# Kernel optimization log

Hardware: AMD Instinct MI355X
Metric: run time of the kernel (lower is better)

## Reference

```python
import jax, jax.numpy as jnp
import numpy as np

B, S, E, H, F = 4, 1024, 1024, 16, 4096
D = E // H
DEPTH = 3
EPS_LN = 1e-5
EPS_ENT = 1e-6


def setup_inputs() -> dict:
    key = jax.random.key(0)
    ks = jax.random.split(key, 32)
    def w(k, shp, s=0.02):
        return (jax.random.normal(k, shp) * s).astype(jnp.float32)
    z = lambda *shp: jnp.zeros(shp, jnp.float32)
    inp = {
        'x': jax.random.normal(ks[0], (B, S, E), jnp.float32),
        # self-referential attention
        'sr_w': w(ks[1], (E, E)), 'sr_b': z(E),
        'q_w': w(ks[2], (E, E)), 'q_b': z(E),
        'k_w': w(ks[3], (E, E)), 'k_b': z(E),
        'v_w': w(ks[4], (E, E)), 'v_b': z(E),
        'o_w': w(ks[5], (E, E)), 'o_b': z(E),
        'ref_gate': jnp.float32(0.5),
        # quantum-classical interface
        'c_w': w(ks[6], (E, E)), 'c_b': z(E),
        'qp_w': w(ks[7], (E, E)), 'qp_b': z(E),
        'ig_w': w(ks[8], (2 * E, E)), 'ig_b': z(E),
        'temperature': jnp.float32(1.0),
        # entropy regulator
        'kp_w': w(ks[9], (E, E)), 'kp_b': z(E),
        'ee_w': w(ks[10], (E, 1)), 'ee_b': z(1),
        'eta': jnp.float32(0.1),
        # ffn
        'f1_w': w(ks[11], (E, F)), 'f1_b': z(F),
        'f2_w': w(ks[12], (F, E)), 'f2_b': z(E),
        # layernorms
        'ln1_g': jnp.ones(E, jnp.float32), 'ln1_b': z(E),
        'ln2_g': jnp.ones(E, jnp.float32), 'ln2_b': z(E),
        'ln3_g': jnp.ones(E, jnp.float32), 'ln3_b': z(E),
        # observer
        'obs_w': w(ks[13], (E, E)), 'obs_b': z(E),
        'obs_gate': jnp.float32(0.2),
    }
    return inp


def _lin(x, W, b):
    return x @ W + b


def _ln(x, g, b):
    m = jnp.mean(x, -1, keepdims=True)
    v = jnp.var(x, -1, keepdims=True)
    return (x - m) * jax.lax.rsqrt(v + EPS_LN) * g + b


def _layer(x, p):
    ks = jax.lax.stop_gradient(x)  # knowledge_state = x.detach()
    scale = 1.0 / (D ** 0.5)
    for _ in range(DEPTH):  # fixed small recursion depth
        # --- self-referential attention on norm1(x) ---
        xn = _ln(x, p['ln1_g'], p['ln1_b'])
        xr = xn + p['ref_gate'] * _lin(xn, p['sr_w'], p['sr_b'])
        b, s, _ = xn.shape
        q = _lin(xr, p['q_w'], p['q_b']).reshape(b, s, H, D)
        k = _lin(xr, p['k_w'], p['k_b']).reshape(b, s, H, D)
        v = _lin(xn, p['v_w'], p['v_b']).reshape(b, s, H, D)
        scores = jnp.einsum('bqhd,bkhd->bhqk', q, k) * scale  # [B,H,S,S]
        aw = jax.nn.softmax(scores, axis=-1)
        ao = jnp.einsum('bhqk,bkhd->bqhd', aw, v).reshape(b, s, E)
        quantum = _lin(ao, p['o_w'], p['o_b'])
        # --- FFN on norm2(x) (dropout = identity, eval mode) ---
        xn2 = _ln(x, p['ln2_g'], p['ln2_b'])
        h = jax.nn.gelu(_lin(xn2, p['f1_w'], p['f1_b']), approximate=False)
        classical = _lin(h, p['f2_w'], p['f2_b'])
        # --- quantum-classical interface ---
        c_proj = _lin(classical, p['c_w'], p['c_b'])
        q_proj = _lin(quantum, p['qp_w'], p['qp_b'])
        gate = jax.nn.sigmoid(_lin(jnp.concatenate([c_proj, q_proj], -1), p['ig_w'], p['ig_b']))
        sim = jnp.einsum('bqe,bke->bqk', c_proj, q_proj) / (E ** 0.5)  # [B,S,S]
        attw = jax.nn.softmax(sim / p['temperature'], axis=-1)
        transfer = jnp.einsum('bqk,bke->bqe', attw, quantum)
        iface = classical + gate * transfer
        # --- entropy regulator ---
        logp = jax.nn.log_softmax(iface, axis=-1)
        entropy = -jnp.sum(jnp.exp(logp) * logp, -1, keepdims=True)
        neg_entropy = _lin(ks, p['kp_w'], p['kp_b'])
        bal = jax.nn.sigmoid(_lin(iface, p['ee_w'], p['ee_b']))
        regulated = iface + p['eta'] * bal * (neg_entropy / (entropy + EPS_ENT))
        # --- residual + observer feedback + knowledge update ---
        x = x + regulated
        x = x + p['obs_gate'] * _lin(x, p['obs_w'], p['obs_b'])
        ks = ks + 0.1 * (x - ks)
    x = _ln(x, p['ln3_g'], p['ln3_b'])
    return x, ks


def reference(x, sr_w, sr_b, q_w, q_b, k_w, k_b, v_w, v_b, o_w, o_b, ref_gate,
              c_w, c_b, qp_w, qp_b, ig_w, ig_b, temperature,
              kp_w, kp_b, ee_w, ee_b, eta,
              f1_w, f1_b, f2_w, f2_b,
              ln1_g, ln1_b, ln2_g, ln2_b, ln3_g, ln3_b,
              obs_w, obs_b, obs_gate):
    p = dict(sr_w=sr_w, sr_b=sr_b, q_w=q_w, q_b=q_b, k_w=k_w, k_b=k_b,
             v_w=v_w, v_b=v_b, o_w=o_w, o_b=o_b, ref_gate=ref_gate,
             c_w=c_w, c_b=c_b, qp_w=qp_w, qp_b=qp_b, ig_w=ig_w, ig_b=ig_b,
             temperature=temperature, kp_w=kp_w, kp_b=kp_b, ee_w=ee_w, ee_b=ee_b,
             eta=eta, f1_w=f1_w, f1_b=f1_b, f2_w=f2_w, f2_b=f2_b,
             ln1_g=ln1_g, ln1_b=ln1_b, ln2_g=ln2_g, ln2_b=ln2_b,
             ln3_g=ln3_g, ln3_b=ln3_b, obs_w=obs_w, obs_b=obs_b, obs_gate=obs_gate)
    return _layer(x, p)
```

## Files before the change

kernel.cpp:

```cpp
#include <hip/hip_runtime.h>
#include <hip/hip_bf16.h>
#include <cmath>


typedef unsigned short u16;
typedef short v8s __attribute__((ext_vector_type(8)));
typedef float v4f __attribute__((ext_vector_type(4)));
typedef unsigned short u16x4 __attribute__((ext_vector_type(4)));

#define DEV __device__ __forceinline__

DEV float b2f(u16 u) { return __uint_as_float(((unsigned int)u) << 16); }
DEV u16 f2b(float f) {
    unsigned int x = __float_as_uint(f);
    return (u16)((x + 0x7fffu + ((x >> 16) & 1u)) >> 16);
}
DEV bool badf(float f) { return ((__float_as_uint(f) >> 23) & 0xFF) == 0xFF; }

DEV void async16(const void* g, void* l) {
    __builtin_amdgcn_global_load_lds((const __attribute__((address_space(1))) void*)g,
                                     (__attribute__((address_space(3))) void*)l, 16, 0, 0);
}

struct InArr { const void* p[37]; int n[37]; };
struct BJobs { int si[20]; int off[20]; int n[20]; };
struct GJ2 { const u16* jA; const u16* jB; const u16* jbias; u16* jout; };

#define CLS_CAP 131072

__global__ void reset_k(int* diag, int* cnt) {
    if (threadIdx.x == 0) *diag = 0x7FFFFFFF;
    if (threadIdx.x < 80) cnt[threadIdx.x] = 0;
}

__global__ void classify_k(InArr A, int* cnt) {
    int i = blockIdx.y;
    int n = A.n[i];
    if (n <= 1) return;
    const u16* q = (const u16*)A.p[i];
    long pairs = n >> 1;
    int wild = 0, pz = 0;
    if (pairs > (long)CLS_CAP) {
        long chunk = CLS_CAP / gridDim.x;
        long p0 = (long)blockIdx.x * (pairs / gridDim.x);
        for (long j = p0 + threadIdx.x; j < p0 + chunk; j += blockDim.x) {
            u16 w0 = q[2 * j], w1 = q[2 * j + 1];
            wild += ((w0 & 0x7FFF) >= 0x5000) + ((w1 & 0x7FFF) >= 0x5000);
            pz += (w0 == 0 && w1 >= 0x3000 && w1 <= 0x4100) ? 1 : 0;
        }
    } else {
        long stride = (long)gridDim.x * blockDim.x;
        for (long j = (long)blockIdx.x * blockDim.x + threadIdx.x; j < pairs; j += stride) {
            u16 w0 = q[2 * j], w1 = q[2 * j + 1];
            wild += ((w0 & 0x7FFF) >= 0x5000) + ((w1 & 0x7FFF) >= 0x5000);
            pz += (w0 == 0 && w1 >= 0x3000 && w1 <= 0x4100) ? 1 : 0;
        }
    }
#pragma unroll
    for (int off = 1; off < 64; off <<= 1) {
        wild += __shfl_xor(wild, off);
        pz += __shfl_xor(pz, off);
    }
    if ((threadIdx.x & 63) == 0) {
        atomicAdd(&cnt[2 * i], wild);
        atomicAdd(&cnt[2 * i + 1], pz);
    }
}

__global__ void finalize_k(InArr A, const int* cnt, int* flags) {
    int i = threadIdx.x;
    if (i < 37) {
        int n = A.n[i];
        int f = 0;
        if (n > 1) {
            long pairs = (long)n >> 1;
            long wthr, pthr;
            if (pairs > (long)CLS_CAP) { wthr = (2L * CLS_CAP) >> 6; pthr = (long)CLS_CAP >> 2; }
            else { wthr = (long)n >> 6; pthr = (long)n >> 3; }
            f = (cnt[2 * i] > wthr) || (cnt[2 * i + 1] > pthr);
        }
        flags[i] = f;
    }
}

DEV float dec_scalar(const u16* p) {
    float bf = b2f(p[0]);
    if (bf > 0.0009765625f && bf < 8.0f) return bf;
    unsigned int w = (((unsigned int)p[1]) << 16) | (unsigned int)p[0];
    return __uint_as_float(w);
}

__global__ void decode_scalars_k(const u16* rg, const u16* tp, const u16* et,
                                 const u16* og, float* out)
{
    if (threadIdx.x == 0 && blockIdx.x == 0) {
        out[0] = dec_scalar(rg);
        out[1] = dec_scalar(tp);
        out[2] = dec_scalar(et);
        out[3] = dec_scalar(og);
    }
}

__global__ void cvt1d_k(InArr A, BJobs J, const int* flags, u16* BIA) {
    int j = blockIdx.y;
    int n = J.n[j];
    int si = J.si[j];
    const void* src = A.p[si];
    u16* dst = BIA + (long)J.off[j] * 1024;
    int f = flags[si];
    int stride = gridDim.x * blockDim.x;
    for (int i = blockIdx.x * blockDim.x + threadIdx.x; i < n; i += stride) {
        dst[i] = f ? f2b(((const float*)src)[i]) : ((const u16*)src)[i];
    }
}

__global__ void chk_scal_k(const float* scal, int* diag) {
    if (threadIdx.x == 0) {
        for (int i = 0; i < 4; i++) {
            float v = scal[i];
            if (!(v > 0.f && v < 8.f)) atomicMin(diag, 3);
        }
    }
}

__global__ void fin32_k(float* out, long n4, const int* diag) {
    long stride = (long)gridDim.x * blockDim.x;
    long i0 = (long)blockIdx.x * blockDim.x + threadIdx.x;
    v4f* o4 = (v4f*)out;
    for (long i = i0; i < n4; i += stride) {
        v4f v = o4[i];
        bool b = false;
#pragma unroll
        for (int j = 0; j < 4; j++) b |= badf(v[j]);
        if (b) {
#pragma unroll
            for (int j = 0; j < 4; j++) if (badf(v[j])) v[j] = 0.f;
            o4[i] = v;
        }
    }
    if (i0 == 0) {
        int d = *diag;
        if (d != 0x7FFFFFFF) out[0] = 200.f + 4.f * (float)(d < 70 ? d : 70);
    }
}

__global__ void small_k(float* out, int code) {
    if (threadIdx.x == 0 && blockIdx.x == 0) out[0] = 900.f + 4.f * code;
}

__global__ __launch_bounds__(256) void f2c_k(const float* __restrict__ a, const float* __restrict__ b,
                                             const u16* __restrict__ bias, u16* __restrict__ out,
                                             int stage, int* __restrict__ diag)
{
    long i0 = ((long)blockIdx.x * 256 + threadIdx.x) * 4;
    v4f va = *(const v4f*)(a + i0);
    v4f vb = *(const v4f*)(b + i0);
    int colb = (int)(i0 & 1023);
    bool bad = false;
    u16x4 o;
#pragma unroll
    for (int j = 0; j < 4; j++) {
        float r = va[j] + vb[j] + b2f(bias[colb + j]);
        bad |= badf(r);
        o[j] = f2b(r);
    }
    *(u16x4*)(out + i0) = o;
    if (__ballot(bad) && (threadIdx.x & 63) == 0) atomicMin(diag, stage);
}

__global__ __launch_bounds__(256) void igc_k(const float* __restrict__ a, const float* __restrict__ b,
                                             const u16* __restrict__ bias, u16* __restrict__ out,
                                             int stage, int* __restrict__ diag)
{
    long i0 = ((long)blockIdx.x * 256 + threadIdx.x) * 4;
    v4f va = *(const v4f*)(a + i0);
    v4f vb = *(const v4f*)(b + i0);
    int colb = (int)(i0 & 1023);
    bool bad = false;
    u16x4 o;
#pragma unroll
    for (int j = 0; j < 4; j++) {
        float r = 1.f / (1.f + expf(-(va[j] + vb[j] + b2f(bias[colb + j]))));
        bad |= badf(r);
        o[j] = f2b(r);
    }
    *(u16x4*)(out + i0) = o;
    if (__ballot(bad) && (threadIdx.x & 63) == 0) atomicMin(diag, stage);
}

template <int EPI>
__global__ __launch_bounds__(512) void gemm_bt(
    const u16* __restrict__ A, int lda, long sA,
    const u16* __restrict__ A2, int ksplit,
    const u16* __restrict__ Bt, int ldb, long sB,
    const u16* __restrict__ bias,
    u16* __restrict__ obf, float* __restrict__ of32, int ldc, long sC,
    int K,
    const float* __restrict__ scp,
    const u16* __restrict__ aux,
    float* __restrict__ xaux, float* __restrict__ ksf, u16* __restrict__ ksb,
    float* __restrict__ kso,
    GJ2 J2,
    int stage, int* __restrict__ diag)
{
    __shared__ __align__(16) u16 As[128 * 64];
    __shared__ __align__(16) u16 Bs[128 * 64];
    const int tid = threadIdx.x;
    const int w = tid >> 6, l = tid & 63;
    const int lr = l & 15, lq = l >> 4;

    const int gx = gridDim.x, gy = gridDim.y;
    const int nwg = gx * gy * (int)gridDim.z;
    int flat = blockIdx.x + gx * (blockIdx.y + gy * blockIdx.z);
    int qq = nwg >> 3, rr = nwg & 7;
    int xcd = flat & 7, loc = flat >> 3;
    int nf = (xcd < rr ? xcd * (qq + 1) : rr * (qq + 1) + (xcd - rr) * qq) + loc;
    const int bx = nf % gx;
    int tmp = nf / gx;
    const int by = tmp % gy;
    int z = tmp / gy;

    const u16* Aj = A; const u16* Bj = Bt; const u16* biasj = bias; u16* obfj = obf;
    float* of32j = of32;
    if (J2.jA) {
        int jzs = (int)gridDim.z >> 1;
        if (z >= jzs) {
            Aj = J2.jA; Bj = J2.jB; biasj = J2.jbias;
            if (EPI == 8) of32j = (float*)J2.jout; else obfj = J2.jout;
            z -= jzs;
        }
    }

    const int m0 = by * 128, n0 = bx * 128;
    const u16* Az = Aj + (long)z * sA;
    const u16* Bz = Bj + (long)z * sB;
    const int wm = (w >> 2) * 64, wn = (w & 3) * 32;

    v4f zero4 = {0.f, 0.f, 0.f, 0.f};
    v4f acc[4][2];
#pragma unroll
    for (int i = 0; i < 4; i++)
#pragma unroll
        for (int j = 0; j < 2; j++) acc[i][j] = zero4;

    const int swz = lr & 7;
    const int c0s = (lq ^ swz) << 3;
    const int c1s = ((lq + 4) ^ swz) << 3;
    for (int k0 = 0; k0 < K; k0 += 64) {
        __syncthreads();
        const u16* Ab = (k0 < ksplit) ? (Az + k0) : (A2 + (k0 - ksplit));
#pragma unroll
        for (int p = 0; p < 2; p++) {
            int c = p * 512 + tid;
            int row = c >> 3;
            int sc = ((c & 7) ^ (row & 7)) * 8;
            async16(Ab + (long)(m0 + row) * lda + sc, (char*)As + p * 8192 + w * 1024);
            async16(Bz + (long)(n0 + row) * ldb + k0 + sc, (char*)Bs + p * 8192 + w * 1024);
        }
        __syncthreads();
        v8s av0[4], av1[4], bv0[2], bv1[2];
#pragma unroll
        for (int mi = 0; mi < 4; mi++) {
            const u16* Ar = As + ((wm + mi * 16 + lr) << 6);
            av0[mi] = *(const v8s*)(Ar + c0s);
            av1[mi] = *(const v8s*)(Ar + c1s);
        }
#pragma unroll
        for (int ni = 0; ni < 2; ni++) {
            const u16* Br = Bs + ((wn + ni * 16 + lr) << 6);
            bv0[ni] = *(const v8s*)(Br + c0s);
            bv1[ni] = *(const v8s*)(Br + c1s);
        }
#pragma unroll
        for (int mi = 0; mi < 4; mi++)
#pragma unroll
            for (int ni = 0; ni < 2; ni++)
                acc[mi][ni] = __builtin_amdgcn_mfma_f32_16x16x32_bf16(av0[mi], bv0[ni], acc[mi][ni], 0, 0, 0);
#pragma unroll
        for (int mi = 0; mi < 4; mi++)
#pragma unroll
            for (int ni = 0; ni < 2; ni++)
                acc[mi][ni] = __builtin_amdgcn_mfma_f32_16x16x32_bf16(av1[mi], bv1[ni], acc[mi][ni], 0, 0, 0);
    }

    float gsv = 0.f;
    if (EPI == 5 || EPI == 6) gsv = scp[0];
    bool bad = false;
#pragma unroll
    for (int mi = 0; mi < 4; mi++) {
        int row = m0 + wm + mi * 16 + lq * 4;
#pragma unroll
        for (int ni = 0; ni < 2; ni++) {
            int col = n0 + wn + ni * 16 + lr;
            float bb = biasj ? b2f(biasj[col]) : 0.f;
#pragma unroll
            for (int r = 0; r < 4; r++) {
                float v = acc[mi][ni][r] + bb;
                if (EPI == 6 || EPI == 7) {
                    long rbase = (long)(row + r) * 1024;
                    float res;
                    if (col < 1024) {
                        if (EPI == 6) res = b2f(aux[rbase + col]) + gsv * v;
                        else res = v * 0.125f;
                        bad |= badf(res);
                        obfj[rbase + col] = f2b(res);
                    } else {
                        res = v;
                        bad |= badf(res);
                        J2.jout[rbase + col - 1024] = f2b(res);
                    }
                } else {
                    long idx = (long)z * sC + (long)(row + r) * ldc + col;
                    float res = v;
                    if (EPI == 2) res = 0.5f * v * (1.f + erff(v * 0.70710678118654752f));
                    else if (EPI == 5) {
                        float xv = xaux[idx];
                        float nx = xv + gsv * v;
                        xaux[idx] = nx;
                        float kv = ksf[idx];
                        float kn = kv + 0.1f * (nx - kv);
                        ksf[idx] = kn;
                        ksb[idx] = f2b(kn);
                        if (kso) kso[idx] = kn;
                        bad |= badf(kn);
                        res = nx;
                    }
                    bad |= badf(res);
                    if (obfj) obfj[idx] = f2b(res);
                    if (of32j) of32j[idx] = res;
                }
            }
        }
    }
    if (__ballot(bad) && l == 0) atomicMin(diag, stage);
}

__global__ __launch_bounds__(256) void flash_k(
    const u16* __restrict__ q, const u16* __restrict__ k, const u16* __restrict__ v,
    u16* __restrict__ ao, int stage, int* __restrict__ diag)
{
    __shared__ __align__(16) u16 Ks[2 * 64 * 64];
    __shared__ __align__(16) u16 Vt[64 * 64];
    __shared__ __align__(16) u16 Pw[4 * 16 * 64];
    const int tid = threadIdx.x, w = tid >> 6, l = tid & 63;
    const int lr = l & 15, lq = l >> 4;
    const int flat = blockIdx.x + (blockIdx.y << 4);
    const int xcd = flat & 7, loc = flat >> 3;
    const int bh = xcd * 8 + (loc >> 4);
    const int q0 = (loc & 15) * 64;
    const int b = bh >> 4, h = bh & 15;
    const long rowbase = (long)b * 1024;
    const int h64 = h * 64;

    const u16* Qp = q + (rowbase + q0 + w * 16 + lr) * 1024 + h64;
    v8s aq0 = *(const v8s*)(Qp + lq * 8);
    v8s aq1 = *(const v8s*)(Qp + 32 + lq * 8);

    v4f zero4 = {0.f, 0.f, 0.f, 0.f};
    v4f oacc[4];
    float m_r[4], l_r[4];
#pragma unroll
    for (int i = 0; i < 4; i++) { oacc[i] = zero4; m_r[i] = -INFINITY; l_r[i] = 0.f; }

    const int ss = lr & 7;
    const int colk = (lq ^ ss) << 3;
    u16* Pp = Pw + w * (16 * 64);

    const int c0 = tid, c1 = 256 + tid;
    const int row0 = c0 >> 3, cc0 = (c0 & 7) * 8;
    const int row1 = c1 >> 3, cc1 = (c1 & 7) * 8;
    const int sl0 = ((c0 & 7) ^ (row0 & 7)) * 8;
    const int sl1 = ((c1 & 7) ^ (row1 & 7)) * 8;
    int vt0[8], vt1[8];
#pragma unroll
    for (int j = 0; j < 8; j++) {
        int d0 = cc0 + j, g0 = (d0 & 7) ^ ((d0 >> 3) & 7);
        vt0[j] = ((d0 << 6) + row0) ^ (g0 << 3);
        int d1 = cc1 + j, g1 = (d1 & 7) ^ ((d1 >> 3) & 7);
        vt1[j] = ((d1 << 6) + row1) ^ (g1 << 3);
    }
    const u16* kc0 = k + (rowbase + row0) * 1024 + h64 + sl0;
    const u16* kc1 = k + (rowbase + row1) * 1024 + h64 + sl1;
    const u16* vc0 = v + (rowbase + row0) * 1024 + h64 + cc0;
    const u16* vc1 = v + (rowbase + row1) * 1024 + h64 + cc1;

    async16(kc0, (char*)Ks + w * 1024);
    async16(kc1, (char*)Ks + 4096 + w * 1024);
    v8s vv0 = *(const v8s*)vc0;
    v8s vv1 = *(const v8s*)vc1;
    v8s vvn0 = vv0, vvn1 = vv1;
    int cur = 0;

    for (int kt = 0; kt < 16; kt++) {
        __syncthreads();
        const long koff = (long)(kt + 1) << 16;
        if (kt < 15) {
            int nb = (cur ^ 1) * 8192;
            async16(kc0 + koff, (char*)Ks + nb + w * 1024);
            async16(kc1 + koff, (char*)Ks + nb + 4096 + w * 1024);
            vvn0 = *(const v8s*)(vc0 + koff);
            vvn1 = *(const v8s*)(vc1 + koff);
        }
        const u16* Kb = Ks + cur * 4096;

        v4f s[4];
#pragma unroll
        for (int nt = 0; nt < 4; nt++) {
            const u16* Kr = Kb + ((nt * 16 + lr) << 6);
            v8s b0 = *(const v8s*)(Kr + colk);
            v8s b1 = *(const v8s*)(Kr + (colk ^ 32));
            v4f t = zero4;
            t = __builtin_amdgcn_mfma_f32_16x16x32_bf16(aq0, b0, t, 0, 0, 0);
            t = __builtin_amdgcn_mfma_f32_16x16x32_bf16(aq1, b1, t, 0, 0, 0);
            s[nt] = t;
        }
#pragma unroll
        for (int r = 0; r < 4; r++) {
            float mx = fmaxf(fmaxf(s[0][r], s[1][r]), fmaxf(s[2][r], s[3][r]));
#pragma unroll
            for (int off = 1; off < 16; off <<= 1) mx = fmaxf(mx, __shfl_xor(mx, off));
            float mn = fmaxf(m_r[r], mx);
            float al = __expf(m_r[r] - mn);
            float rs = 0.f;
            int qrow = lq * 4 + r;
            int pbase = qrow << 6;
            int pswz = (qrow & 7) << 3;
#pragma unroll
            for (int nt = 0; nt < 4; nt++) {
                float pv = __expf(s[nt][r] - mn);
                rs += pv;
                Pp[pbase + ((nt * 16 + lr) ^ pswz)] = f2b(pv);
            }
#pragma unroll
            for (int off = 1; off < 16; off <<= 1) rs += __shfl_xor(rs, off);
            l_r[r] = l_r[r] * al + rs;
            m_r[r] = mn;
#pragma unroll
            for (int nt = 0; nt < 4; nt++) oacc[nt][r] *= al;
        }
#pragma unroll
        for (int j = 0; j < 8; j++) {
            Vt[vt0[j]] = (u16)vv0[j];
            Vt[vt1[j]] = (u16)vv1[j];
        }
        __syncthreads();
        const u16* Pr = Pp + (lr << 6);
        v8s pa0 = *(const v8s*)(Pr + colk);
        v8s pa1 = *(const v8s*)(Pr + (colk ^ 32));
#pragma unroll
        for (int nt = 0; nt < 4; nt++) {
            const u16* Vr = Vt + ((nt * 16 + lr) << 6);
            int gv = (ss ^ (2 * nt + (lr >> 3))) << 3;
            int colv = (lq << 3) ^ gv;
            v8s vb0 = *(const v8s*)(Vr + colv);
            v8s vb1 = *(const v8s*)(Vr + (colv ^ 32));
            oacc[nt] = __builtin_amdgcn_mfma_f32_16x16x32_bf16(pa0, vb0, oacc[nt], 0, 0, 0);
            oacc[nt] = __builtin_amdgcn_mfma_f32_16x16x32_bf16(pa1, vb1, oacc[nt], 0, 0, 0);
        }
        vv0 = vvn0; vv1 = vvn1;
        cur ^= 1;
    }
    bool bad = false;
#pragma unroll
    for (int r = 0; r < 4; r++) {
        float inv = 1.f / l_r[r];
#pragma unroll
        for (int nt = 0; nt < 4; nt++) {
            float val = oacc[nt][r] * inv;
            bad |= badf(val);
            ao[(rowbase + q0 + w * 16 + lq * 4 + r) * 1024 + h64 + nt * 16 + lr] = f2b(val);
        }
    }
    if (__ballot(bad) && l == 0) atomicMin(diag, stage);
}

template <int F32OUT>
__global__ __launch_bounds__(256) void ln_k(const float* __restrict__ x,
                                            const u16* __restrict__ g, const u16* __restrict__ bt,
                                            u16* __restrict__ outb, float* __restrict__ outf,
                                            int stage, int* __restrict__ diag)
{
    __shared__ float red[8];
    int row = blockIdx.x, t = threadIdx.x, w = t >> 6;
    const float* xr = x + (long)row * 1024;
    float v[4], s = 0.f, sq = 0.f;
#pragma unroll
    for (int i = 0; i < 4; i++) { v[i] = xr[i * 256 + t]; s += v[i]; sq += v[i] * v[i]; }
#pragma unroll
    for (int off = 1; off < 64; off <<= 1) { s += __shfl_xor(s, off); sq += __shfl_xor(sq, off); }
    if ((t & 63) == 0) { red[w] = s; red[4 + w] = sq; }
    __syncthreads();
    float S = red[0] + red[1] + red[2] + red[3];
    float SQ = red[4] + red[5] + red[6] + red[7];
    float mean = S * (1.f / 1024.f);
    float var = fmaxf(SQ * (1.f / 1024.f) - mean * mean, 0.f);
    float rs = rsqrtf(var + 1e-5f);
    bool bad = false;
#pragma unroll
    for (int i = 0; i < 4; i++) {
        int e = i * 256 + t;
        float r = (v[i] - mean) * rs * b2f(g[e]) + b2f(bt[e]);
        bad |= badf(r);
        if (F32OUT) outf[(long)row * 1024 + e] = r;
        else outb[(long)row * 1024 + e] = f2b(r);
    }
    if (__ballot(bad) && (t & 63) == 0) atomicMin(diag, stage);
}

__global__ __launch_bounds__(256) void ln12_k(const float* __restrict__ x,
                                              const u16* __restrict__ g1, const u16* __restrict__ b1,
                                              const u16* __restrict__ g2, const u16* __restrict__ b2,
                                              u16* __restrict__ out1, u16* __restrict__ out2,
                                              int stage, int* __restrict__ diag)
{
    __shared__ float red[8];
    int row = blockIdx.x, t = threadIdx.x, w = t >> 6;
    const float* xr = x + (long)row * 1024;
    float v[4], s = 0.f, sq = 0.f;
#pragma unroll
    for (int i = 0; i < 4; i++) { v[i] = xr[i * 256 + t]; s += v[i]; sq += v[i] * v[i]; }
#pragma unroll
    for (int off = 1; off < 64; off <<= 1) { s += __shfl_xor(s, off); sq += __shfl_xor(sq, off); }
    if ((t & 63) == 0) { red[w] = s; red[4 + w] = sq; }
    __syncthreads();
    float S = red[0] + red[1] + red[2] + red[3];
    float SQ = red[4] + red[5] + red[6] + red[7];
    float mean = S * (1.f / 1024.f);
    float var = fmaxf(SQ * (1.f / 1024.f) - mean * mean, 0.f);
    float rs = rsqrtf(var + 1e-5f);
    bool bad = false;
#pragma unroll
    for (int i = 0; i < 4; i++) {
        int e = i * 256 + t;
        float nv = (v[i] - mean) * rs;
        float r1 = nv * b2f(g1[e]) + b2f(b1[e]);
        float r2 = nv * b2f(g2[e]) + b2f(b2[e]);
        bad |= badf(r1) | badf(r2);
        out1[(long)row * 1024 + e] = f2b(r1);
        out2[(long)row * 1024 + e] = f2b(r2);
    }
    if (__ballot(bad) && (t & 63) == 0) atomicMin(diag, stage);
}

__global__ __launch_bounds__(256) void rowfuse_k(
    const u16* __restrict__ cls, const u16* __restrict__ gate,
    const float* __restrict__ tra, const float* __restrict__ trb,
    const u16* __restrict__ ne, const u16* __restrict__ eew, const u16* __restrict__ eeb,
    const float* __restrict__ eta_p, float* __restrict__ xbuf, u16* __restrict__ x1b,
    int stage, int* __restrict__ diag)
{
    __shared__ float red[16];
    int row = blockIdx.x, t = threadIdx.x, w = t >> 6;
    long base = (long)row * 1024;
    float ifc[4];
#pragma unroll
    for (int i = 0; i < 4; i++) {
        int e = i * 256 + t;
        ifc[i] = b2f(cls[base + e]) + b2f(gate[base + e]) * (tra[base + e] + trb[base + e]);
    }
    float mx = fmaxf(fmaxf(ifc[0], ifc[1]), fmaxf(ifc[2], ifc[3]));
#pragma unroll
    for (int off = 1; off < 64; off <<= 1) mx = fmaxf(mx, __shfl_xor(mx, off));
    if ((t & 63) == 0) red[w] = mx;
    __syncthreads();
    float MX = fmaxf(fmaxf(red[0], red[1]), fmaxf(red[2], red[3]));
    float s1 = 0.f, s2 = 0.f, dot = 0.f;
#pragma unroll
    for (int i = 0; i < 4; i++) {
        int e = i * 256 + t;
        float ex = expf(ifc[i] - MX);
        s1 += ex; s2 += ex * ifc[i]; dot += ifc[i] * b2f(eew[e]);
    }
#pragma unroll
    for (int off = 1; off < 64; off <<= 1) {
        s1 += __shfl_xor(s1, off); s2 += __shfl_xor(s2, off); dot += __shfl_xor(dot, off);
    }
    if ((t & 63) == 0) { red[4 + w] = s1; red[8 + w] = s2; red[12 + w] = dot; }
    __syncthreads();
    float S1 = red[4] + red[5] + red[6] + red[7];
    float S2 = red[8] + red[9] + red[10] + red[11];
    float DT = red[12] + red[13] + red[14] + red[15];
    float logZ = MX + logf(S1);
    float ent = logZ - S2 / S1;
    float bal = 1.f / (1.f + expf(-(DT + b2f(eeb[0]))));
    float fac = eta_p[0] * bal / (ent + 1e-6f);
    bool bad = false;
#pragma unroll
    for (int i = 0; i < 4; i++) {
        int e = i * 256 + t;
        float rg = ifc[i] + fac * b2f(ne[base + e]);
        float x1 = xbuf[base + e] + rg;
        bad |= badf(x1);
        xbuf[base + e] = x1;
        x1b[base + e] = f2b(x1);
    }
    if (__ballot(bad) && (t & 63) == 0) atomicMin(diag, stage);
}

__global__ __launch_bounds__(256) void softmax_k(const float* __restrict__ pa, const float* __restrict__ pb,
                                                 const float* __restrict__ tp, u16* __restrict__ out,
                                                 int stage, int* __restrict__ diag)
{
    __shared__ float red[8];
    int row = blockIdx.x, t = threadIdx.x, w = t >> 6;
    long base = (long)row * 1024;
    float sc = 0.03125f / fmaxf(tp[0], 1e-8f);
    float v[4];
#pragma unroll
    for (int i = 0; i < 4; i++) v[i] = (pa[base + i * 256 + t] + pb[base + i * 256 + t]) * sc;
    float mx = fmaxf(fmaxf(v[0], v[1]), fmaxf(v[2], v[3]));
#pragma unroll
    for (int off = 1; off < 64; off <<= 1) mx = fmaxf(mx, __shfl_xor(mx, off));
    if ((t & 63) == 0) red[w] = mx;
    __syncthreads();
    float MX = fmaxf(fmaxf(red[0], red[1]), fmaxf(red[2], red[3]));
    float s = 0.f;
#pragma unroll
    for (int i = 0; i < 4; i++) { v[i] = expf(v[i] - MX); s += v[i]; }
#pragma unroll
    for (int off = 1; off < 64; off <<= 1) s += __shfl_xor(s, off);
    if ((t & 63) == 0) red[4 + w] = s;
    __syncthreads();
    float inv = 1.f / (red[4] + red[5] + red[6] + red[7]);
    bool bad = false;
#pragma unroll
    for (int i = 0; i < 4; i++) {
        float o = v[i] * inv;
        bad |= badf(o);
        out[base + i * 256 + t] = f2b(o);
    }
    if (__ballot(bad) && (t & 63) == 0) atomicMin(diag, stage);
}

__global__ void transpose_ft_k(const void* __restrict__ in, u16* __restrict__ out,
                               int R, int C, const int* __restrict__ flags, int idx,
                               int* __restrict__ diag)
{
    __shared__ u16 tile[32][33];
    int f = flags[idx];
    int x = blockIdx.x * 32 + threadIdx.x;
    int y0 = blockIdx.y * 32;
#pragma unroll
    for (int j = 0; j < 4; j++) {
        long src = (long)(y0 + threadIdx.y + j * 8) * C + x;
        tile[threadIdx.y + j * 8][threadIdx.x] =
            f ? f2b(((const float*)in)[src]) : ((const u16*)in)[src];
    }
    __syncthreads();
    int ox = y0 + threadIdx.x;
    int oy0 = blockIdx.x * 32;
    bool bad = false;
#pragma unroll
    for (int j = 0; j < 4; j++) {
        u16 u = tile[threadIdx.x][threadIdx.y + j * 8];
        bad |= ((u & 0x7FFF) >= 0x7F80);
        out[(long)(oy0 + threadIdx.y + j * 8) * R + ox] = u;
    }
    if (__ballot(bad) && ((threadIdx.y * 32 + threadIdx.x) & 63) == 0) atomicMin(diag, 2);
}

__global__ void transpose_k(const u16* __restrict__ in, u16* __restrict__ out,
                            int R, int C, long sIn, long sOut)
{
    __shared__ u16 tile[32][33];
    int z = blockIdx.z;
    in += (long)z * sIn; out += (long)z * sOut;
    int x = blockIdx.x * 32 + threadIdx.x;
    int y0 = blockIdx.y * 32;
#pragma unroll
    for (int j = 0; j < 4; j++)
        tile[threadIdx.y + j * 8][threadIdx.x] = in[(long)(y0 + threadIdx.y + j * 8) * C + x];
    __syncthreads();
    int ox = y0 + threadIdx.x;
    int oy0 = blockIdx.x * 32;
#pragma unroll
    for (int j = 0; j < 4; j++)
        out[(long)(oy0 + threadIdx.y + j * 8) * R + ox] = tile[threadIdx.x][threadIdx.y + j * 8];
}

__global__ __launch_bounds__(256) void init_k(const void* __restrict__ xin, const int* __restrict__ flags,
                                              float* __restrict__ xbuf,
                                              float* __restrict__ ksf, u16* __restrict__ ksb,
                                              int* __restrict__ diag)
{
    int t = threadIdx.x;
    int f = flags[0];
    long base = (long)blockIdx.x * 1024;
    bool bad = false;
#pragma unroll
    for (int i = 0; i < 4; i++) {
        long idx = base + i * 256 + t;
        float xv = f ? ((const float*)xin)[idx] : b2f(((const u16*)xin)[idx]);
        bad |= badf(xv);
        xbuf[idx] = xv; ksf[idx] = xv; ksb[idx] = f2b(xv);
    }
    if (__ballot(bad) && (t & 63) == 0) atomicMin(diag, 1);
}

extern "C" void kernel_launch(void* const* d_in, const int* in_sizes, int n_in,
                              void* d_out, int out_size, void* d_ws, size_t ws_size,
                              hipStream_t stream)
{
    const size_t MB = 1u << 20;
    float* outf = (float*)d_out;
    if (ws_size < 192 * MB) {
        int code = (int)(ws_size >> 25); if (code > 9) code = 9;
        small_k<<<1, 64, 0, stream>>>(outf, code);
        return;
    }
    const u16* s_refg = (const u16*)d_in[11];
    const u16* s_temp = (const u16*)d_in[18];
    const u16* s_eta  = (const u16*)d_in[23];
    const u16* s_obsg = (const u16*)d_in[36];

    InArr IA;
    for (int i = 0; i < 37; i++) { IA.p[i] = d_in[i]; IA.n[i] = (i < n_in) ? in_sizes[i] : 0; }

    char* ws = (char*)d_ws;
    u16* srT  = (u16*)(ws + 0 * MB);
    u16* vT   = (u16*)(ws + 2 * MB);
    u16* qT   = (u16*)(ws + 4 * MB);
    u16* kT   = (u16*)(ws + 6 * MB);
    u16* oT   = (u16*)(ws + 8 * MB);
    u16* cT   = (u16*)(ws + 10 * MB);
    u16* qpT  = (u16*)(ws + 12 * MB);
    u16* kpT  = (u16*)(ws + 14 * MB);
    u16* obsT = (u16*)(ws + 16 * MB);
    u16* igT  = (u16*)(ws + 18 * MB);
    u16* f1T  = (u16*)(ws + 22 * MB);
    u16* f2T  = (u16*)(ws + 30 * MB);
    float* scal = (float*)(ws + 38 * MB);
    int* diag  = (int*)(ws + 38 * MB + 64);
    int* flags = (int*)(ws + 38 * MB + 128);
    int* cnt   = (int*)(ws + 38 * MB + 512);
    u16* BIA   = (u16*)(ws + 38 * MB + 8192);
    u16* c_bsr = BIA + 0*1024,  *c_bv = BIA + 1*1024;
    u16* c_bq  = BIA + 2*1024,  *c_bk = BIA + 3*1024;
    u16* c_bo  = BIA + 4*1024,  *c_bc = BIA + 5*1024;
    u16* c_bqp = BIA + 6*1024,  *c_big = BIA + 7*1024, *c_bkp = BIA + 8*1024;
    u16* c_bobs= BIA + 9*1024,  *c_bf2 = BIA + 10*1024;
    u16* c_g1  = BIA + 11*1024, *c_be1 = BIA + 12*1024;
    u16* c_g2  = BIA + 13*1024, *c_be2 = BIA + 14*1024;
    u16* c_g3  = BIA + 15*1024, *c_be3 = BIA + 16*1024;
    u16* c_eew = BIA + 17*1024, *c_eeb = BIA + 18*1024;
    u16* c_bf1 = BIA + 19*1024;
    float* xbuf = (float*)(ws + 40 * MB);
    float* ksf  = (float*)(ws + 56 * MB);
    u16* ksb    = (u16*)(ws + 72 * MB);
    u16* xn     = (u16*)(ws + 80 * MB);
    u16* xn2    = (u16*)(ws + 88 * MB);
    u16* xr     = (u16*)(ws + 96 * MB);
    u16* qb     = (u16*)(ws + 104 * MB);
    u16* kb     = (u16*)(ws + 112 * MB);
    u16* vb     = (u16*)(ws + 120 * MB);
    u16* aob    = (u16*)(ws + 128 * MB);
    u16* quant  = (u16*)(ws + 136 * MB);
    u16* hb     = (u16*)(ws + 144 * MB);
    u16* clsb   = (u16*)(ws + 176 * MB);
    u16* neb    = (u16*)(ws + 184 * MB);
    float* f2pa = (float*)(ws + 104 * MB);
    float* f2pb = (float*)(ws + 120 * MB);
    float* ppa  = (float*)(ws + 144 * MB);
    float* ppb  = (float*)(ws + 160 * MB);
    u16* quantT = xn;
    u16* cpb = qb;  u16* qpb = kb;  u16* gateb = vb;  u16* attw = aob;  u16* x1b = xr;

    const long BS1 = 1024L * 1024L;
    const int KBIG = 1 << 30;
    dim3 tb(32, 8), blk(256), gblk(512);
    GJ2 J0 = {nullptr, nullptr, nullptr, nullptr};

    auto G = [&](int epi, int gx, int gy, int gz,
                 const u16* A, int lda, long sA, const u16* A2, int ksp,
                 const u16* Bt, int ldb, long sB, const u16* bias,
                 u16* obf, float* of32, int ldc, long sC, int K,
                 const float* scp, const u16* aux, float* xa, float* kf, u16* kb2, float* kso,
                 GJ2 J2, int stg) {
        dim3 grid(gx, gy, gz);
        switch (epi) {
            case 0: gemm_bt<0><<<grid, gblk, 0, stream>>>(A, lda, sA, A2, ksp, Bt, ldb, sB, bias, obf, of32, ldc, sC, K, scp, aux, xa, kf, kb2, kso, J2, stg, diag); break;
            case 2: gemm_bt<2><<<grid, gblk, 0, stream>>>(A, lda, sA, A2, ksp, Bt, ldb, sB, bias, obf, of32, ldc, sC, K, scp, aux, xa, kf, kb2, kso, J2, stg, diag); break;
            case 5: gemm_bt<5><<<grid, gblk, 0, stream>>>(A, lda, sA, A2, ksp, Bt, ldb, sB, bias, obf, of32, ldc, sC, K, scp, aux, xa, kf, kb2, kso, J2, stg, diag); break;
            case 6: gemm_bt<6><<<grid, gblk, 0, stream>>>(A, lda, sA, A2, ksp, Bt, ldb, sB, bias, obf, of32, ldc, sC, K, scp, aux, xa, kf, kb2, kso, J2, stg, diag); break;
            case 7: gemm_bt<7><<<grid, gblk, 0, stream>>>(A, lda, sA, A2, ksp, Bt, ldb, sB, bias, obf, of32, ldc, sC, K, scp, aux, xa, kf, kb2, kso, J2, stg, diag); break;
            case 8: gemm_bt<8><<<grid, gblk, 0, stream>>>(A, lda, sA, A2, ksp, Bt, ldb, sB, bias, obf, of32, ldc, sC, K, scp, aux, xa, kf, kb2, kso, J2, stg, diag); break;
        }
    };

    reset_k<<<1, 256, 0, stream>>>(diag, cnt);
    classify_k<<<dim3(64, 37), blk, 0, stream>>>(IA, cnt);
    finalize_k<<<1, 64, 0, stream>>>(IA, cnt, flags);
    decode_scalars_k<<<1, 64, 0, stream>>>(s_refg, s_temp, s_eta, s_obsg, scal);
    BJobs BJ = {
        {2, 8, 4, 6, 10, 13, 15, 17, 20, 35, 27, 28, 29, 30, 31, 32, 33, 21, 22, 25},
        {0, 1, 2, 3, 4, 5, 6, 7, 8, 9, 10, 11, 12, 13, 14, 15, 16, 17, 18, 19},
        {1024,1024,1024,1024,1024,1024,1024,1024,1024,1024,1024,1024,1024,1024,1024,1024,1024,1024,1,4096}
    };
    cvt1d_k<<<dim3(4, 20), blk, 0, stream>>>(IA, BJ, flags, BIA);
    struct WT { int idx; u16* dst; long n; int R, C, gx, gy; };
    WT wts[12] = {
        {1, srT, 1048576, 1024, 1024, 32, 32},  {7, vT, 1048576, 1024, 1024, 32, 32},
        {3, qT, 1048576, 1024, 1024, 32, 32},   {5, kT, 1048576, 1024, 1024, 32, 32},
        {9, oT, 1048576, 1024, 1024, 32, 32},   {12, cT, 1048576, 1024, 1024, 32, 32},
        {14, qpT, 1048576, 1024, 1024, 32, 32}, {19, kpT, 1048576, 1024, 1024, 32, 32},
        {34, obsT, 1048576, 1024, 1024, 32, 32},
        {16, igT, 2097152, 2048, 1024, 32, 64},
        {24, f1T, 4194304, 1024, 4096, 128, 32},
        {26, f2T, 4194304, 4096, 1024, 32, 128},
    };
    for (int i = 0; i < 12; i++) {
        transpose_ft_k<<<dim3(wts[i].gx, wts[i].gy, 1), tb, 0, stream>>>(
            d_in[wts[i].idx], wts[i].dst, wts[i].R, wts[i].C, flags, wts[i].idx, diag);
    }
    init_k<<<4096, blk, 0, stream>>>(d_in[0], flags, xbuf, ksf, ksb, diag);
    chk_scal_k<<<1, 64, 0, stream>>>(scal, diag);

    for (int it = 0; it < 3; it++) {
        int sb = 4 + it * 20;
        ln12_k<<<4096, blk, 0, stream>>>(xbuf, c_g1, c_be1, c_g2, c_be2, xn, xn2, sb + 0, diag);
        GJ2 Jsrv = {nullptr, nullptr, nullptr, vb};
        G(6, 16, 32, 1, xn, 1024, 0, nullptr, KBIG, srT, 1024, 0, c_bsr, xr, nullptr, 1024, 0, 1024, scal + 0, xn, nullptr, nullptr, nullptr, nullptr, Jsrv, sb + 1);
        GJ2 Jqk = {nullptr, nullptr, nullptr, kb};
        G(7, 16, 32, 1, xr, 1024, 0, nullptr, KBIG, qT, 1024, 0, c_bq, qb, nullptr, 1024, 0, 1024, nullptr, nullptr, nullptr, nullptr, nullptr, nullptr, Jqk, sb + 2);
        flash_k<<<dim3(16, 64), blk, 0, stream>>>(qb, kb, vb, aob, sb + 5, diag);
        GJ2 Jokp = {ksb, kpT, c_bkp, neb};
        G(0, 8, 32, 2, aob, 1024, 0, nullptr, KBIG, oT, 1024, 0, c_bo, quant, nullptr, 1024, 0, 1024, nullptr, nullptr, nullptr, nullptr, nullptr, nullptr, Jokp, sb + 6);
        transpose_k<<<dim3(32, 32, 4), tb, 0, stream>>>(quant, quantT, 1024, 1024, BS1, BS1);
        G(2, 32, 32, 1, xn2, 1024, 0, nullptr, KBIG, f1T, 1024, 0, c_bf1, hb, nullptr, 4096, 0, 1024, nullptr, nullptr, nullptr, nullptr, nullptr, nullptr, J0, sb + 8);
        G(8, 8, 32, 2, hb, 4096, 2048, nullptr, KBIG, f2T, 4096, 2048, nullptr, nullptr, f2pa, 1024, 4194304, 2048, nullptr, nullptr, nullptr, nullptr, nullptr, nullptr, J0, sb + 9);
        f2c_k<<<4096, blk, 0, stream>>>(f2pa, f2pb, c_bf2, clsb, sb + 9, diag);
        GJ2 Jcqp = {quant, qpT, c_bqp, qpb};
        G(0, 8, 32, 2, clsb, 1024, 0, nullptr, KBIG, cT, 1024, 0, c_bc, cpb, nullptr, 1024, 0, 1024, nullptr, nullptr, nullptr, nullptr, nullptr, nullptr, Jcqp, sb + 10);
        GJ2 Jig = {qpb, igT + 1024, nullptr, (u16*)ppb};
        G(8, 8, 32, 2, cpb, 1024, 0, nullptr, KBIG, igT, 2048, 0, nullptr, nullptr, ppa, 1024, 0, 1024, nullptr, nullptr, nullptr, nullptr, nullptr, nullptr, Jig, sb + 12);
        igc_k<<<4096, blk, 0, stream>>>(ppa, ppb, c_big, gateb, sb + 12, diag);
        GJ2 Jsim = {cpb + 512, qpb + 512, nullptr, (u16*)ppb};
        G(8, 8, 8, 8, cpb, 1024, BS1, nullptr, KBIG, qpb, 1024, BS1, nullptr, nullptr, ppa, 1024, BS1, 512, nullptr, nullptr, nullptr, nullptr, nullptr, nullptr, Jsim, sb + 14);
        softmax_k<<<4096, blk, 0, stream>>>(ppa, ppb, scal + 1, attw, sb + 15, diag);
        GJ2 Jtrf = {attw + 512, quantT + 512, nullptr, (u16*)ppb};
        G(8, 8, 8, 8, attw, 1024, BS1, nullptr, KBIG, quantT, 1024, BS1, nullptr, nullptr, ppa, 1024, BS1, 512, nullptr, nullptr, nullptr, nullptr, nullptr, nullptr, Jtrf, sb + 16);
        rowfuse_k<<<4096, blk, 0, stream>>>(clsb, gateb, ppa, ppb, neb, c_eew, c_eeb, scal + 2, xbuf, x1b, sb + 17, diag);
        float* kso = (it == 2) ? (outf + 4194304) : nullptr;
        G(5, 8, 32, 1, x1b, 1024, 0, nullptr, KBIG, obsT, 1024, 0, c_bobs, nullptr, nullptr, 1024, 0, 1024, scal + 3, nullptr, xbuf, ksf, ksb, kso, J0, sb + 18);
    }
    ln_k<1><<<4096, blk, 0, stream>>>(xbuf, c_g3, c_be3, nullptr, outf, 70, diag);
    fin32_k<<<1024, blk, 0, stream>>>(outf, 2097152, diag);
}
```

Measured before the change: 1.647 ms.

## Split flash attention over the KV dimension with a separate combine kernel

Flash attention now splits the 1024-key range into two halves across a third grid dimension, doubling the block count from 1024 to 2048. Each half writes unnormalised fp32 partial outputs plus per-row max and sum to workspace. A new elementwise kernel merges the two partials with a log-sum-exp rescale and writes the bf16 attention output. This aims to raise occupancy and parallelism on the many-CU GPU. In exchange it adds fp32 partial traffic (about 32MB written and read) and an extra launch.

```diff
diff --git a/kernel.cpp b/kernel.cpp
--- a/kernel.cpp
+++ b/kernel.cpp
@@ -185,6 +185,34 @@
         o[j] = f2b(r);
     }
     *(u16x4*)(out + i0) = o;
+    if (__ballot(bad) && (threadIdx.x & 63) == 0) atomicMin(diag, stage);
+}
+
+__global__ __launch_bounds__(256) void flashc_k(
+    const float* __restrict__ Of, const float* __restrict__ Mf, const float* __restrict__ Lf,
+    u16* __restrict__ ao, int stage, int* __restrict__ diag)
+{
+    long i0 = ((long)blockIdx.x * 256 + threadIdx.x) * 4;
+    int row4 = (int)(i0 >> 10);
+    int col = (int)(i0 & 1023);
+    int b = row4 >> 10, srow = row4 & 1023, h = col >> 6;
+    int mli = (((b << 4) + h) << 10) + srow;
+    float m0 = Mf[mli], m1 = Mf[65536 + mli];
+    float l0 = Lf[mli], l1 = Lf[65536 + mli];
+    float m = fmaxf(m0, m1);
+    float e0 = __expf(m0 - m), e1 = __expf(m1 - m);
+    float inv = 1.f / (l0 * e0 + l1 * e1);
+    v4f a = *(const v4f*)(Of + i0);
+    v4f bb = *(const v4f*)(Of + 4194304 + i0);
+    bool bad = false;
+    u16x4 o;
+#pragma unroll
+    for (int j = 0; j < 4; j++) {
+        float val = (a[j] * e0 + bb[j] * e1) * inv;
+        bad |= badf(val);
+        o[j] = f2b(val);
+    }
+    *(u16x4*)(ao + i0) = o;
     if (__ballot(bad) && (threadIdx.x & 63) == 0) atomicMin(diag, stage);
 }
 
@@ -337,20 +365,23 @@
 
 __global__ __launch_bounds__(256) void flash_k(
     const u16* __restrict__ q, const u16* __restrict__ k, const u16* __restrict__ v,
-    u16* __restrict__ ao, int stage, int* __restrict__ diag)
+    float* __restrict__ Of, float* __restrict__ Mf, float* __restrict__ Lf)
 {
     __shared__ __align__(16) u16 Ks[2 * 64 * 64];
     __shared__ __align__(16) u16 Vt[64 * 64];
     __shared__ __align__(16) u16 Pw[4 * 16 * 64];
     const int tid = threadIdx.x, w = tid >> 6, l = tid & 63;
     const int lr = l & 15, lq = l >> 4;
-    const int flat = blockIdx.x + (blockIdx.y << 4);
+    const int flat = blockIdx.x + (blockIdx.y << 4) + (blockIdx.z << 10);
     const int xcd = flat & 7, loc = flat >> 3;
-    const int bh = xcd * 8 + (loc >> 4);
-    const int q0 = (loc & 15) * 64;
+    const int bh = xcd * 8 + (loc >> 5);
+    const int rest = loc & 31;
+    const int zk = rest >> 4;
+    const int q0 = (rest & 15) * 64;
     const int b = bh >> 4, h = bh & 15;
     const long rowbase = (long)b * 1024;
     const int h64 = h * 64;
+    const long zoff = (long)zk << 19;
 
     const u16* Qp = q + (rowbase + q0 + w * 16 + lr) * 1024 + h64;
     v8s aq0 = *(const v8s*)(Qp + lq * 8);
@@ -379,10 +410,10 @@
         int d1 = cc1 + j, g1 = (d1 & 7) ^ ((d1 >> 3) & 7);
         vt1[j] = ((d1 << 6) + row1) ^ (g1 << 3);
     }
-    const u16* kc0 = k + (rowbase + row0) * 1024 + h64 + sl0;
-    const u16* kc1 = k + (rowbase + row1) * 1024 + h64 + sl1;
-    const u16* vc0 = v + (rowbase + row0) * 1024 + h64 + cc0;
-    const u16* vc1 = v + (rowbase + row1) * 1024 + h64 + cc1;
+    const u16* kc0 = k + (rowbase + row0) * 1024 + h64 + sl0 + zoff;
+    const u16* kc1 = k + (rowbase + row1) * 1024 + h64 + sl1 + zoff;
+    const u16* vc0 = v + (rowbase + row0) * 1024 + h64 + cc0 + zoff;
+    const u16* vc1 = v + (rowbase + row1) * 1024 + h64 + cc1 + zoff;
 
     async16(kc0, (char*)Ks + w * 1024);
     async16(kc1, (char*)Ks + 4096 + w * 1024);
@@ -391,10 +422,10 @@
     v8s vvn0 = vv0, vvn1 = vv1;
     int cur = 0;
 
-    for (int kt = 0; kt < 16; kt++) {
+    for (int kt = 0; kt < 8; kt++) {
         __syncthreads();
         const long koff = (long)(kt + 1) << 16;
-        if (kt < 15) {
+        if (kt < 7) {
             int nb = (cur ^ 1) * 8192;
             async16(kc0 + koff, (char*)Ks + nb + w * 1024);
             async16(kc1 + koff, (char*)Ks + nb + 4096 + w * 1024);
@@ -460,18 +491,20 @@
         vv0 = vvn0; vv1 = vvn1;
         cur ^= 1;
     }
-    bool bad = false;
+    float* Ofz = Of + (long)zk * 4194304;
 #pragma unroll
     for (int r = 0; r < 4; r++) {
-        float inv = 1.f / l_r[r];
+        int srow = q0 + w * 16 + lq * 4 + r;
 #pragma unroll
         for (int nt = 0; nt < 4; nt++) {
-            float val = oacc[nt][r] * inv;
-            bad |= badf(val);
-            ao[(rowbase + q0 + w * 16 + lq * 4 + r) * 1024 + h64 + nt * 16 + lr] = f2b(val);
-        }
-    }
-    if (__ballot(bad) && l == 0) atomicMin(diag, stage);
+            Ofz[(rowbase + srow) * 1024 + h64 + nt * 16 + lr] = oacc[nt][r];
+        }
+        if (lr == 0) {
+            int mli = zk * 65536 + (bh << 10) + srow;
+            Mf[mli] = m_r[r];
+            Lf[mli] = l_r[r];
+        }
+    }
 }
 
 template <int F32OUT>
@@ -744,6 +777,8 @@
     u16* c_g3  = BIA + 15*1024, *c_be3 = BIA + 16*1024;
     u16* c_eew = BIA + 17*1024, *c_eeb = BIA + 18*1024;
     u16* c_bf1 = BIA + 19*1024;
+    float* Mf = (float*)(ws + 39 * MB);
+    float* Lf = (float*)(ws + 39 * MB + 524288);
     float* xbuf = (float*)(ws + 40 * MB);
     float* ksf  = (float*)(ws + 56 * MB);
     u16* ksb    = (u16*)(ws + 72 * MB);
@@ -822,7 +857,8 @@
         G(6, 16, 32, 1, xn, 1024, 0, nullptr, KBIG, srT, 1024, 0, c_bsr, xr, nullptr, 1024, 0, 1024, scal + 0, xn, nullptr, nullptr, nullptr, nullptr, Jsrv, sb + 1);
         GJ2 Jqk = {nullptr, nullptr, nullptr, kb};
         G(7, 16, 32, 1, xr, 1024, 0, nullptr, KBIG, qT, 1024, 0, c_bq, qb, nullptr, 1024, 0, 1024, nullptr, nullptr, nullptr, nullptr, nullptr, nullptr, Jqk, sb + 2);
-        flash_k<<<dim3(16, 64), blk, 0, stream>>>(qb, kb, vb, aob, sb + 5, diag);
+        flash_k<<<dim3(16, 64, 2), blk, 0, stream>>>(qb, kb, vb, ppa, Mf, Lf);
+        flashc_k<<<4096, blk, 0, stream>>>(ppa, Mf, Lf, aob, sb + 5, diag);
         GJ2 Jokp = {ksb, kpT, c_bkp, neb};
         G(0, 8, 32, 2, aob, 1024, 0, nullptr, KBIG, oT, 1024, 0, c_bo, quant, nullptr, 1024, 0, 1024, nullptr, nullptr, nullptr, nullptr, nullptr, nullptr, Jokp, sb + 6);
         transpose_k<<<dim3(32, 32, 4), tb, 0, stream>>>(quant, quantT, 1024, 1024, BS1, BS1);
```

Result: no change. 1.650 ms (+0.2%).

## Double-buffer GEMM LDS tiles with K=32 steps and shrink input classification sampling

Applied to the files above, without the earlier changes.

The GEMM main loop switches from a single 64-wide K tile with two barriers per step to a double-buffered 32-wide K tile. The next tile's async global-to-LDS load is issued before the MFMAs on the current tile, so load latency can overlap compute, and the LDS swizzle is rewritten for the 32-column layout. Separately, the input-format classifier samples fewer elements with vectorized 16-byte loads and a smaller grid, cutting its fixed overhead. The risks are more loop iterations and barriers per unit of K, plus a possibly weaker classification heuristic from the smaller sample.

```diff
diff --git a/kernel.cpp b/kernel.cpp
--- a/kernel.cpp
+++ b/kernel.cpp
@@ -7,6 +7,7 @@
 typedef short v8s __attribute__((ext_vector_type(8)));
 typedef float v4f __attribute__((ext_vector_type(4)));
 typedef unsigned short u16x4 __attribute__((ext_vector_type(4)));
+typedef unsigned int u32x4 __attribute__((ext_vector_type(4)));
 
 #define DEV __device__ __forceinline__
 
@@ -26,7 +27,7 @@
 struct BJobs { int si[20]; int off[20]; int n[20]; };
 struct GJ2 { const u16* jA; const u16* jB; const u16* jbias; u16* jout; };
 
-#define CLS_CAP 131072
+#define CLS_CAP 16384
 
 __global__ void reset_k(int* diag, int* cnt) {
     if (threadIdx.x == 0) *diag = 0x7FFFFFFF;
@@ -37,18 +38,25 @@
     int i = blockIdx.y;
     int n = A.n[i];
     if (n <= 1) return;
-    const u16* q = (const u16*)A.p[i];
-    long pairs = n >> 1;
+    long pairs = (long)n >> 1;
     int wild = 0, pz = 0;
-    if (pairs > (long)CLS_CAP) {
-        long chunk = CLS_CAP / gridDim.x;
-        long p0 = (long)blockIdx.x * (pairs / gridDim.x);
-        for (long j = p0 + threadIdx.x; j < p0 + chunk; j += blockDim.x) {
-            u16 w0 = q[2 * j], w1 = q[2 * j + 1];
-            wild += ((w0 & 0x7FFF) >= 0x5000) + ((w1 & 0x7FFF) >= 0x5000);
-            pz += (w0 == 0 && w1 >= 0x3000 && w1 <= 0x4100) ? 1 : 0;
+    if (pairs > (long)(2 * CLS_CAP)) {
+        const unsigned int* q32 = (const unsigned int*)A.p[i];
+        long p0 = ((long)blockIdx.x * (pairs >> 3)) & ~3L;
+        long tbase = p0 + (long)threadIdx.x * 8;
+#pragma unroll
+        for (int c = 0; c < 2; c++) {
+            u32x4 v = *(const u32x4*)(q32 + tbase + c * 4);
+#pragma unroll
+            for (int j = 0; j < 4; j++) {
+                unsigned int p = v[j];
+                u16 w0 = (u16)(p & 0xFFFFu), w1 = (u16)(p >> 16);
+                wild += ((w0 & 0x7FFF) >= 0x5000) + ((w1 & 0x7FFF) >= 0x5000);
+                pz += (w0 == 0 && w1 >= 0x3000 && w1 <= 0x4100) ? 1 : 0;
+            }
         }
     } else {
+        const u16* q = (const u16*)A.p[i];
         long stride = (long)gridDim.x * blockDim.x;
         for (long j = (long)blockIdx.x * blockDim.x + threadIdx.x; j < pairs; j += stride) {
             u16 w0 = q[2 * j], w1 = q[2 * j + 1];
@@ -75,7 +83,7 @@
         if (n > 1) {
             long pairs = (long)n >> 1;
             long wthr, pthr;
-            if (pairs > (long)CLS_CAP) { wthr = (2L * CLS_CAP) >> 6; pthr = (long)CLS_CAP >> 2; }
+            if (pairs > (long)(2 * CLS_CAP)) { wthr = (2L * CLS_CAP) >> 6; pthr = (long)CLS_CAP >> 2; }
             else { wthr = (long)n >> 6; pthr = (long)n >> 3; }
             f = (cnt[2 * i] > wthr) || (cnt[2 * i + 1] > pthr);
         }
@@ -203,8 +211,8 @@
     GJ2 J2,
     int stage, int* __restrict__ diag)
 {
-    __shared__ __align__(16) u16 As[128 * 64];
-    __shared__ __align__(16) u16 Bs[128 * 64];
+    __shared__ __align__(16) u16 As[2 * 128 * 32];
+    __shared__ __align__(16) u16 Bs[2 * 128 * 32];
     const int tid = threadIdx.x;
     const int w = tid >> 6, l = tid & 63;
     const int lr = l & 15, lq = l >> 4;
@@ -243,44 +251,41 @@
 #pragma unroll
         for (int j = 0; j < 2; j++) acc[i][j] = zero4;
 
-    const int swz = lr & 7;
-    const int c0s = (lq ^ swz) << 3;
-    const int c1s = ((lq + 4) ^ swz) << 3;
-    for (int k0 = 0; k0 < K; k0 += 64) {
+    const int cslot = (lq ^ ((lr >> 1) & 3)) << 3;
+    const int srow = tid >> 2;
+    const int ssc = (((tid & 3) ^ ((srow >> 1) & 3)) * 8);
+
+    {
+        const u16* Ab = (0 < ksplit) ? Az : A2;
+        async16(Ab + (long)(m0 + srow) * lda + ssc, (char*)As + w * 1024);
+        async16(Bz + (long)(n0 + srow) * ldb + ssc, (char*)Bs + w * 1024);
+    }
+    __syncthreads();
+    int cur = 0;
+    for (int k0 = 0; k0 < K; k0 += 32) {
+        int kn = k0 + 32;
+        if (kn < K) {
+            const u16* Ab = (kn < ksplit) ? (Az + kn) : (A2 + (kn - ksplit));
+            int nb = (cur ^ 1) * 8192;
+            async16(Ab + (long)(m0 + srow) * lda + ssc, (char*)As + nb + w * 1024);
+            async16(Bz + (long)(n0 + srow) * ldb + kn + ssc, (char*)Bs + nb + w * 1024);
+        }
+        const u16* Asc = As + cur * 4096;
+        const u16* Bsc = Bs + cur * 4096;
+        v8s av[4], bv[2];
+#pragma unroll
+        for (int mi = 0; mi < 4; mi++)
+            av[mi] = *(const v8s*)(Asc + ((wm + mi * 16 + lr) << 5) + cslot);
+#pragma unroll
+        for (int ni = 0; ni < 2; ni++)
+            bv[ni] = *(const v8s*)(Bsc + ((wn + ni * 16 + lr) << 5) + cslot);
+#pragma unroll
+        for (int mi = 0; mi < 4; mi++)
+#pragma unroll
+            for (int ni = 0; ni < 2; ni++)
+                acc[mi][ni] = __builtin_amdgcn_mfma_f32_16x16x32_bf16(av[mi], bv[ni], acc[mi][ni], 0, 0, 0);
         __syncthreads();
-        const u16* Ab = (k0 < ksplit) ? (Az + k0) : (A2 + (k0 - ksplit));
-#pragma unroll
-        for (int p = 0; p < 2; p++) {
-            int c = p * 512 + tid;
-            int row = c >> 3;
-            int sc = ((c & 7) ^ (row & 7)) * 8;
-            async16(Ab + (long)(m0 + row) * lda + sc, (char*)As + p * 8192 + w * 1024);
-            async16(Bz + (long)(n0 + row) * ldb + k0 + sc, (char*)Bs + p * 8192 + w * 1024);
-        }
-        __syncthreads();
-        v8s av0[4], av1[4], bv0[2], bv1[2];
-#pragma unroll
-        for (int mi = 0; mi < 4; mi++) {
-            const u16* Ar = As + ((wm + mi * 16 + lr) << 6);
-            av0[mi] = *(const v8s*)(Ar + c0s);
-            av1[mi] = *(const v8s*)(Ar + c1s);
-        }
-#pragma unroll
-        for (int ni = 0; ni < 2; ni++) {
-            const u16* Br = Bs + ((wn + ni * 16 + lr) << 6);
-            bv0[ni] = *(const v8s*)(Br + c0s);
-            bv1[ni] = *(const v8s*)(Br + c1s);
-        }
-#pragma unroll
-        for (int mi = 0; mi < 4; mi++)
-#pragma unroll
-            for (int ni = 0; ni < 2; ni++)
-                acc[mi][ni] = __builtin_amdgcn_mfma_f32_16x16x32_bf16(av0[mi], bv0[ni], acc[mi][ni], 0, 0, 0);
-#pragma unroll
-        for (int mi = 0; mi < 4; mi++)
-#pragma unroll
-            for (int ni = 0; ni < 2; ni++)
-                acc[mi][ni] = __builtin_amdgcn_mfma_f32_16x16x32_bf16(av1[mi], bv1[ni], acc[mi][ni], 0, 0, 0);
+        cur ^= 1;
     }
 
     float gsv = 0.f;
@@ -788,7 +793,7 @@
     };
 
     reset_k<<<1, 256, 0, stream>>>(diag, cnt);
-    classify_k<<<dim3(64, 37), blk, 0, stream>>>(IA, cnt);
+    classify_k<<<dim3(8, 37), blk, 0, stream>>>(IA, cnt);
     finalize_k<<<1, 64, 0, stream>>>(IA, cnt, flags);
     decode_scalars_k<<<1, 64, 0, stream>>>(s_refg, s_temp, s_eta, s_obsg, scal);
     BJobs BJ = {
```

Measured after the change: 1.645 ms. Within noise of the previous version (-0.1%).
